# Optimization experiments

Hardware: AMD Instinct MI355X
Metric: run time of the kernel (lower is better)

Reference implementation:

```python
import jax, jax.numpy as jnp
import numpy as np


def _apply_rope(t, cos, sin):
    # t: [b, s, h, d]; cos/sin: [s, d//2]; interleaved complex rotation
    b, s, h, d = t.shape
    tr = t.reshape(b, s, h, d // 2, 2)
    a, bb = tr[..., 0], tr[..., 1]
    c = cos[None, :, None, :]
    si = sin[None, :, None, :]
    out_r = a * c - bb * si
    out_i = a * si + bb * c
    return jnp.stack([out_r, out_i], axis=-1).reshape(b, s, h, d)


def setup_inputs() -> dict:
    key = jax.random.key(0)
    ks = jax.random.split(key, 10)
    B, S, D = 4, 512, 4096
    H, HKV, HD = 32, 8, 128
    START = 512
    wscale = 0.02  # keep activations in sane range
    x = jax.random.normal(ks[0], (B, S, D), dtype=jnp.float32)
    wq = jax.random.normal(ks[1], (H * HD, D), dtype=jnp.float32) * wscale
    wk = jax.random.normal(ks[2], (HKV * HD, D), dtype=jnp.float32) * wscale
    wv = jax.random.normal(ks[3], (HKV * HD, D), dtype=jnp.float32) * wscale
    wo = jax.random.normal(ks[4], (D, H * HD), dtype=jnp.float32) * wscale
    # RoPE angles for absolute positions [START, START+S)
    theta = 500000.0
    inv_freq = 1.0 / (theta ** (np.arange(0, HD, 2, dtype=np.float32) / HD))
    pos = np.arange(START, START + S, dtype=np.float32)
    ang = pos[:, None] * inv_freq[None, :]  # [S, HD//2]
    freqs_cos = jnp.asarray(np.cos(ang), dtype=jnp.float32)
    freqs_sin = jnp.asarray(np.sin(ang), dtype=jnp.float32)
    cache_k = jax.random.normal(ks[5], (B, START, HKV, HD), dtype=jnp.float32)
    cache_v = jax.random.normal(ks[6], (B, START, HKV, HD), dtype=jnp.float32)
    return {"x": x, "wq": wq, "wk": wk, "wv": wv, "wo": wo,
            "freqs_cos": freqs_cos, "freqs_sin": freqs_sin,
            "cache_k": cache_k, "cache_v": cache_v, "start_pos": START}


def reference(x, wq, wk, wv, wo, freqs_cos, freqs_sin, cache_k, cache_v, start_pos):
    B, S, D = x.shape
    H = wq.shape[0] // 128
    HKV = wk.shape[0] // 128
    HD = 128
    n_rep = H // HKV
    # QKV projections (Linear: y = x @ W^T)
    xq = jnp.einsum('bsd,ed->bse', x, wq).reshape(B, S, H, HD)
    xk = jnp.einsum('bsd,ed->bse', x, wk).reshape(B, S, HKV, HD)
    xv = jnp.einsum('bsd,ed->bse', x, wv).reshape(B, S, HKV, HD)
    # rotary embedding on new q/k
    xq = _apply_rope(xq, freqs_cos, freqs_sin)
    xk = _apply_rope(xk, freqs_cos, freqs_sin)
    # append new k/v to cache -> total kv length T = start_pos + S
    keys = jnp.concatenate([cache_k, xk], axis=1)    # [B, T, HKV, HD]
    values = jnp.concatenate([cache_v, xv], axis=1)  # [B, T, HKV, HD]
    # GQA: repeat kv heads (repeat_interleave along head dim)
    keys = jnp.repeat(keys, n_rep, axis=2)      # [B, T, H, HD]
    values = jnp.repeat(values, n_rep, axis=2)  # [B, T, H, HD]
    scores = jnp.einsum('bqhd,bkhd->bhqk', xq, keys) / jnp.sqrt(jnp.float32(HD))
    # causal mask: query abs pos start_pos+i attends to kv pos <= start_pos+i
    T = start_pos + S
    q_pos = start_pos + jnp.arange(S)
    k_pos = jnp.arange(T)
    mask = k_pos[None, :] <= q_pos[:, None]  # [S, T]
    scores = jnp.where(mask[None, None, :, :], scores, -jnp.inf)
    probs = jax.nn.softmax(scores.astype(jnp.float32), axis=-1).astype(x.dtype)
    out = jnp.einsum('bhqk,bkhd->bqhd', probs, values).reshape(B, S, H * HD)
    return jnp.einsum('bse,de->bsd', out, wo)
```

## Files before the change

kernel.cpp:

```cpp
#include <hip/hip_runtime.h>
#include <hip/hip_bf16.h>


#define B_ 4
#define S_ 512
#define D_ 4096
#define H_ 32
#define HKV_ 8
#define HD_ 128
#define T_ 1024
#define M_ 2048
#define NQKV_ 6144

typedef __attribute__((ext_vector_type(8))) short bf16x8;
typedef __attribute__((ext_vector_type(4))) float f32x4;

#define GLOAD_LDS16(g, l)                                                     \
  __builtin_amdgcn_global_load_lds(                                           \
      (const __attribute__((address_space(1))) void*)(g),                     \
      (__attribute__((address_space(3))) void*)(l), 16, 0, 0)

__global__ void cvt_f32_bf16(const float* __restrict__ in,
                             __hip_bfloat16* __restrict__ out, long n) {
  long i = ((long)blockIdx.x * blockDim.x + threadIdx.x) * 4;
  if (i >= n) return;
  float4 v = *(const float4*)(in + i);
  __hip_bfloat16 t[4] = {__float2bfloat16(v.x), __float2bfloat16(v.y),
                         __float2bfloat16(v.z), __float2bfloat16(v.w)};
  *(uint2*)(out + i) = *(const uint2*)t;
}

__global__ __launch_bounds__(512, 2) void gemm_qkv(
    const __hip_bfloat16* __restrict__ A, const __hip_bfloat16* __restrict__ B,
    float* __restrict__ C, int K, long ldA, long ldB, long ldC) {
  const int lin = blockIdx.x + 32 * blockIdx.y;
  const int swz = (lin & 7) * 32 + (lin >> 3);
  const int m0 = (swz >> 5) << 8;
  const int n0 = (swz & 31) * 192;

  const int tid = threadIdx.x;
  const int w = tid >> 6, l = tid & 63;
  const int wm = w >> 2, wn = w & 3;
  const int lr = l & 15, lq = l >> 4;

  __shared__ __align__(16) __hip_bfloat16 smem[2][28672];

  const int rS = w * 8 + (l >> 3);
  const int cS = (l & 7) ^ (l >> 3);
  const __hip_bfloat16* gA = A + (long)(m0 + rS) * ldA + cS * 8;
  const __hip_bfloat16* gB = B + (long)(n0 + rS) * ldB + cS * 8;
  const int wofs = w * 512;

  const int sl0 = (lq ^ (lr & 7)) * 8;
  const int sl1 = ((4 + lq) ^ (lr & 7)) * 8;
  const int aRow = (wm * 128 + lr) * 64;
  const int bRow = (wn * 48 + lr) * 64;

  f32x4 acc[8][3];
#pragma unroll
  for (int i = 0; i < 8; i++)
#pragma unroll
    for (int j = 0; j < 3; j++) acc[i][j] = f32x4{0.f, 0.f, 0.f, 0.f};

  const int nkt = K >> 6;

#define STAGEQ(buf, ko)                                              \
  {                                                                  \
    GLOAD_LDS16(gA + (ko), &smem[buf][wofs]);                        \
    GLOAD_LDS16(gA + 64 * ldA + (ko), &smem[buf][4096 + wofs]);      \
    GLOAD_LDS16(gA + 128 * ldA + (ko), &smem[buf][8192 + wofs]);     \
    GLOAD_LDS16(gA + 192 * ldA + (ko), &smem[buf][12288 + wofs]);    \
    GLOAD_LDS16(gB + (ko), &smem[buf][16384 + wofs]);                \
    GLOAD_LDS16(gB + 64 * ldB + (ko), &smem[buf][20480 + wofs]);     \
    GLOAD_LDS16(gB + 128 * ldB + (ko), &smem[buf][24576 + wofs]);    \
  }

  STAGEQ(0, 0);
  asm volatile("s_waitcnt vmcnt(0)" ::: "memory");
  __builtin_amdgcn_s_barrier();

  bf16x8 af[4], bfr[3];
  for (int t = 0; t < nkt; ++t) {
    const int bc = t & 1;
    int tn = t + 1;
    if (tn == nkt) tn = 0;
    const long ko = (long)tn << 6;
    const __hip_bfloat16* rA = &smem[bc][0];
    const __hip_bfloat16* rB = &smem[bc][16384];

#pragma unroll
    for (int i = 0; i < 4; i++)
      af[i] = *(const bf16x8*)(rA + aRow + i * 1024 + sl0);
#pragma unroll
    for (int j = 0; j < 3; j++)
      bfr[j] = *(const bf16x8*)(rB + bRow + j * 1024 + sl0);
    STAGEQ(bc ^ 1, ko);
    __builtin_amdgcn_s_barrier();
    __builtin_amdgcn_s_setprio(1);
#pragma unroll
    for (int i = 0; i < 4; i++)
#pragma unroll
      for (int j = 0; j < 3; j++)
        acc[i][j] = __builtin_amdgcn_mfma_f32_16x16x32_bf16(af[i], bfr[j],
                                                            acc[i][j], 0, 0, 0);
    __builtin_amdgcn_s_setprio(0);
    __builtin_amdgcn_s_barrier();

#pragma unroll
    for (int i = 0; i < 4; i++)
      af[i] = *(const bf16x8*)(rA + aRow + (i + 4) * 1024 + sl0);
    __builtin_amdgcn_s_barrier();
    __builtin_amdgcn_s_setprio(1);
#pragma unroll
    for (int i = 0; i < 4; i++)
#pragma unroll
      for (int j = 0; j < 3; j++)
        acc[i + 4][j] = __builtin_amdgcn_mfma_f32_16x16x32_bf16(
            af[i], bfr[j], acc[i + 4][j], 0, 0, 0);
    __builtin_amdgcn_s_setprio(0);
    __builtin_amdgcn_s_barrier();

#pragma unroll
    for (int i = 0; i < 4; i++)
      af[i] = *(const bf16x8*)(rA + aRow + i * 1024 + sl1);
#pragma unroll
    for (int j = 0; j < 3; j++)
      bfr[j] = *(const bf16x8*)(rB + bRow + j * 1024 + sl1);
    __builtin_amdgcn_s_barrier();
    __builtin_amdgcn_s_setprio(1);
#pragma unroll
    for (int i = 0; i < 4; i++)
#pragma unroll
      for (int j = 0; j < 3; j++)
        acc[i][j] = __builtin_amdgcn_mfma_f32_16x16x32_bf16(af[i], bfr[j],
                                                            acc[i][j], 0, 0, 0);
    __builtin_amdgcn_s_setprio(0);
    __builtin_amdgcn_s_barrier();

#pragma unroll
    for (int i = 0; i < 4; i++)
      af[i] = *(const bf16x8*)(rA + aRow + (i + 4) * 1024 + sl1);
    __builtin_amdgcn_s_barrier();
    __builtin_amdgcn_s_setprio(1);
#pragma unroll
    for (int i = 0; i < 4; i++)
#pragma unroll
      for (int j = 0; j < 3; j++)
        acc[i + 4][j] = __builtin_amdgcn_mfma_f32_16x16x32_bf16(
            af[i], bfr[j], acc[i + 4][j], 0, 0, 0);
    __builtin_amdgcn_s_setprio(0);
    asm volatile("s_waitcnt vmcnt(0)" ::: "memory");
    __builtin_amdgcn_s_barrier();
  }

#undef STAGEQ

  const int crow = m0 + wm * 128 + lq * 4;
  const int ccol = n0 + wn * 48 + lr;
#pragma unroll
  for (int i = 0; i < 8; i++)
#pragma unroll
    for (int j = 0; j < 3; j++)
#pragma unroll
      for (int r = 0; r < 4; r++)
        C[(long)(crow + i * 16 + r) * ldC + (ccol + j * 16)] = acc[i][j][r];
}

__global__ __launch_bounds__(512, 2) void gemm128(
    const __hip_bfloat16* __restrict__ A, const __hip_bfloat16* __restrict__ B,
    float* __restrict__ C, int M, int N, int K, long ldA, long ldB, long ldC) {
  const int nbx = N >> 8;
  const int nwg = nbx * (M >> 7);
  const int lin = blockIdx.x + nbx * blockIdx.y;
  const int cpx = nwg >> 3;
  const int swz = (lin & 7) * cpx + (lin >> 3);
  const int by = swz / nbx;
  const int m0 = by << 7;
  const int n0 = (swz - by * nbx) << 8;

  const int tid = threadIdx.x;
  const int w = tid >> 6, l = tid & 63;
  const int wm = w >> 2, wn = w & 3;
  const int lr = l & 15, lq = l >> 4;

  __shared__ __align__(16) __hip_bfloat16 smem[3][24576];

  const int rS = w * 16 + (l >> 2);
  const int cS = (l & 3) ^ ((rS >> 1) & 3);
  const __hip_bfloat16* gA = A + (long)(m0 + rS) * ldA + cS * 8;
  const __hip_bfloat16* gB = B + (long)(n0 + rS) * ldB + cS * 8;
  const long stB = 128 * ldB;
  const int wofs = w * 512;

  const int cR = (lq ^ ((lr >> 1) & 3)) * 8;
  const int aOff = (wm * 64 + lr) * 32 + cR;
  const int bOff = (wn * 64 + lr) * 32 + cR;

  f32x4 acc[4][4];
#pragma unroll
  for (int i = 0; i < 4; i++)
#pragma unroll
    for (int j = 0; j < 4; j++) acc[i][j] = f32x4{0.f, 0.f, 0.f, 0.f};

  const int nkt = K >> 6;

#define STAGEF(buf, ko)                                            \
  {                                                                \
    const __hip_bfloat16* ga_ = gA + (ko);                         \
    GLOAD_LDS16(ga_, &smem[buf][wofs]);                            \
    GLOAD_LDS16(ga_ + 32, &smem[buf][4096 + wofs]);                \
    const __hip_bfloat16* gb_ = gB + (ko);                         \
    GLOAD_LDS16(gb_, &smem[buf][8192 + wofs]);                     \
    GLOAD_LDS16(gb_ + stB, &smem[buf][12288 + wofs]);              \
    GLOAD_LDS16(gb_ + 32, &smem[buf][16384 + wofs]);               \
    GLOAD_LDS16(gb_ + stB + 32, &smem[buf][20480 + wofs]);         \
  }

  STAGEF(0, 0);
  STAGEF(1, 64);
  asm volatile("s_waitcnt vmcnt(6)" ::: "memory");
  __builtin_amdgcn_s_barrier();

  int bc = 0, b1 = 1, b2 = 2;
  bf16x8 af[4], bfr[4];
  for (int t = 0; t < nkt; ++t) {
    int t2 = t + 2;
    if (t2 >= nkt) t2 -= nkt;
    const long ko2 = (long)t2 << 6;
    STAGEF(b2, ko2);

    const __hip_bfloat16* rA = &smem[bc][0];
    const __hip_bfloat16* rB = &smem[bc][8192];

#pragma unroll
    for (int i = 0; i < 4; i++) af[i] = *(const bf16x8*)(rA + aOff + i * 512);
#pragma unroll
    for (int j = 0; j < 4; j++) bfr[j] = *(const bf16x8*)(rB + bOff + j * 512);
    __builtin_amdgcn_s_setprio(1);
#pragma unroll
    for (int i = 0; i < 4; i++)
#pragma unroll
      for (int j = 0; j < 4; j++)
        acc[i][j] = __builtin_amdgcn_mfma_f32_16x16x32_bf16(af[i], bfr[j],
                                                            acc[i][j], 0, 0, 0);
    __builtin_amdgcn_s_setprio(0);

#pragma unroll
    for (int i = 0; i < 4; i++)
      af[i] = *(const bf16x8*)(rA + 4096 + aOff + i * 512);
#pragma unroll
    for (int j = 0; j < 4; j++)
      bfr[j] = *(const bf16x8*)(rB + 8192 + bOff + j * 512);
    __builtin_amdgcn_s_setprio(1);
#pragma unroll
    for (int i = 0; i < 4; i++)
#pragma unroll
      for (int j = 0; j < 4; j++)
        acc[i][j] = __builtin_amdgcn_mfma_f32_16x16x32_bf16(af[i], bfr[j],
                                                            acc[i][j], 0, 0, 0);
    __builtin_amdgcn_s_setprio(0);

    asm volatile("s_waitcnt lgkmcnt(0)" ::: "memory");
    __builtin_amdgcn_sched_barrier(0);
    asm volatile("s_waitcnt vmcnt(6)" ::: "memory");
    __builtin_amdgcn_s_barrier();

    int tmp = bc; bc = b1; b1 = b2; b2 = tmp;
  }
  asm volatile("s_waitcnt vmcnt(0)" ::: "memory");

#undef STAGEF

  const int crow = m0 + wm * 64 + lq * 4;
  const int ccol = n0 + wn * 64 + lr;
#pragma unroll
  for (int i = 0; i < 4; i++)
#pragma unroll
    for (int j = 0; j < 4; j++)
#pragma unroll
      for (int r = 0; r < 4; r++)
        C[(long)(crow + i * 16 + r) * ldC + (ccol + j * 16)] = acc[i][j][r];
}

__global__ __launch_bounds__(256, 2) void flash_attn(
    const __hip_bfloat16* __restrict__ qb,
    const __hip_bfloat16* __restrict__ kb,
    const __hip_bfloat16* __restrict__ vtb,
    __hip_bfloat16* __restrict__ ob) {
  const int qt = 3 - blockIdx.x;
  const int z = blockIdx.y;
  const int b = z >> 5, h = z & 31, kvh = h >> 2;
  const int q0 = qt * 128;
  const int tid = threadIdx.x, wave = tid >> 6, lane = tid & 63;
  const int lr = lane & 15, lq = lane >> 4;
  const int wrow = wave * 32;
  const float scale = 0.08838834764831845f;

  __shared__ __align__(16) __hip_bfloat16 smem[64 * 128 + 128 * 64 + 128 * 72];
  __hip_bfloat16* Ks = smem;
  __hip_bfloat16* Vs = smem + 64 * 128;
  __hip_bfloat16* Ps = smem + 64 * 128 + 128 * 64;
  __hip_bfloat16* Os = smem;

  const __hip_bfloat16* Kz = kb + ((long)(b * 8 + kvh)) * T_ * HD_;
  const __hip_bfloat16* Vz = vtb + ((long)(b * 8 + kvh)) * HD_ * T_;
  const __hip_bfloat16* Qz = qb + ((long)(b * 512 + q0)) * 4096 + h * 128;
  __hip_bfloat16* obz = ob + ((long)(b * 512 + q0)) * 4096 + h * 128;

  bf16x8 qf[2][4];
#pragma unroll
  for (int i = 0; i < 2; i++)
#pragma unroll
    for (int kb4 = 0; kb4 < 4; kb4++)
      qf[i][kb4] = *(const bf16x8*)(Qz + (long)(wrow + i * 16 + lr) * 4096 +
                                    kb4 * 32 + lq * 8);

  int kOff[4], vOff[4];
#pragma unroll
  for (int it = 0; it < 4; it++) {
    int G = it * 256 + tid;
    int t = G >> 4, ck = (G & 15) ^ (t & 7);
    kOff[it] = t * 128 + ck * 8;
    int d = G >> 3, cv = (G & 7) ^ (d & 7);
    vOff[it] = d * 1024 + cv * 8;
  }

  f32x4 O[2][8];
#pragma unroll
  for (int i = 0; i < 2; i++)
#pragma unroll
    for (int j = 0; j < 8; j++) O[i][j] = f32x4{0.f, 0.f, 0.f, 0.f};
  float mst[2][4], lst[2][4];
#pragma unroll
  for (int i = 0; i < 2; i++)
#pragma unroll
    for (int r = 0; r < 4; r++) {
      mst[i][r] = -1e30f;
      lst[i][r] = 0.f;
    }

  const int ntiles = 10 + 2 * qt, fulltiles = 8 + 2 * qt;
  const int hxor = lr & 7;

  bf16x8 kreg[4], vreg[4];
#pragma unroll
  for (int it = 0; it < 4; it++)
    kreg[it] = *(const bf16x8*)(Kz + kOff[it]);
#pragma unroll
  for (int it = 0; it < 4; it++)
    vreg[it] = *(const bf16x8*)(Vz + vOff[it]);

  for (int kt = 0; kt < ntiles; kt++) {
    const int k0 = kt * 64;
#pragma unroll
    for (int it = 0; it < 4; it++)
      *(bf16x8*)(Ks + (it * 256 + tid) * 8) = kreg[it];
#pragma unroll
    for (int it = 0; it < 4; it++)
      *(bf16x8*)(Vs + (it * 256 + tid) * 8) = vreg[it];
    if (kt + 1 < ntiles) {
      const long kn = (long)(kt + 1) * 64;
#pragma unroll
      for (int it = 0; it < 4; it++)
        kreg[it] = *(const bf16x8*)(Kz + kn * 128 + kOff[it]);
#pragma unroll
      for (int it = 0; it < 4; it++)
        vreg[it] = *(const bf16x8*)(Vz + kn + vOff[it]);
    }
    asm volatile("s_waitcnt lgkmcnt(0)" ::: "memory");
    __builtin_amdgcn_s_barrier();

    f32x4 s[2][4];
#pragma unroll
    for (int i = 0; i < 2; i++)
#pragma unroll
      for (int j = 0; j < 4; j++) s[i][j] = f32x4{0.f, 0.f, 0.f, 0.f};
#pragma unroll
    for (int kb4 = 0; kb4 < 4; kb4++) {
      bf16x8 kf[4];
#pragma unroll
      for (int j = 0; j < 4; j++)
        kf[j] = *(const bf16x8*)(Ks + (j * 16 + lr) * 128 +
                                 ((kb4 * 4 + lq) ^ hxor) * 8);
#pragma unroll
      for (int i = 0; i < 2; i++)
#pragma unroll
        for (int j = 0; j < 4; j++)
          s[i][j] = __builtin_amdgcn_mfma_f32_16x16x32_bf16(qf[i][kb4], kf[j],
                                                            s[i][j], 0, 0, 0);
    }

    const bool mt = (kt >= fulltiles);
#pragma unroll
    for (int i = 0; i < 2; i++)
#pragma unroll
      for (int j = 0; j < 4; j++)
#pragma unroll
        for (int r = 0; r < 4; r++) {
          float sv = s[i][j][r] * scale;
          if (mt) {
            int key = k0 + j * 16 + lr;
            int qp = 512 + q0 + wrow + i * 16 + lq * 4 + r;
            if (key > qp) sv = -1e30f;
          }
          s[i][j][r] = sv;
        }

    float al[2][4];
#pragma unroll
    for (int i = 0; i < 2; i++)
#pragma unroll
      for (int r = 0; r < 4; r++) {
        float mx = fmaxf(fmaxf(s[i][0][r], s[i][1][r]),
                         fmaxf(s[i][2][r], s[i][3][r]));
        mx = fmaxf(mx, __shfl_xor(mx, 1));
        mx = fmaxf(mx, __shfl_xor(mx, 2));
        mx = fmaxf(mx, __shfl_xor(mx, 4));
        mx = fmaxf(mx, __shfl_xor(mx, 8));
        float mn = fmaxf(mst[i][r], mx);
        al[i][r] = __expf(mst[i][r] - mn);
        mst[i][r] = mn;
      }
#pragma unroll
    for (int i = 0; i < 2; i++)
#pragma unroll
      for (int j = 0; j < 4; j++)
#pragma unroll
        for (int r = 0; r < 4; r++)
          s[i][j][r] = __expf(s[i][j][r] - mst[i][r]);
#pragma unroll
    for (int i = 0; i < 2; i++)
#pragma unroll
      for (int r = 0; r < 4; r++) {
        float sm = s[i][0][r] + s[i][1][r] + s[i][2][r] + s[i][3][r];
        sm += __shfl_xor(sm, 1);
        sm += __shfl_xor(sm, 2);
        sm += __shfl_xor(sm, 4);
        sm += __shfl_xor(sm, 8);
        lst[i][r] = lst[i][r] * al[i][r] + sm;
      }
#pragma unroll
    for (int i = 0; i < 2; i++)
#pragma unroll
      for (int j = 0; j < 8; j++)
#pragma unroll
        for (int r = 0; r < 4; r++) O[i][j][r] *= al[i][r];

#pragma unroll
    for (int i = 0; i < 2; i++)
#pragma unroll
      for (int j = 0; j < 4; j++)
#pragma unroll
        for (int r = 0; r < 4; r++)
          Ps[(wrow + i * 16 + lq * 4 + r) * 72 + j * 16 + lr] =
              __float2bfloat16(s[i][j][r]);

#pragma unroll
    for (int kc = 0; kc < 2; kc++) {
      bf16x8 pa[2];
#pragma unroll
      for (int i = 0; i < 2; i++)
        pa[i] = *(const bf16x8*)(Ps + (wrow + i * 16 + lr) * 72 + kc * 32 +
                                 lq * 8);
      bf16x8 vf[8];
#pragma unroll
      for (int j = 0; j < 8; j++)
        vf[j] = *(const bf16x8*)(Vs + (j * 16 + lr) * 64 +
                                 ((kc * 4 + lq) ^ hxor) * 8);
#pragma unroll
      for (int i = 0; i < 2; i++)
#pragma unroll
        for (int j = 0; j < 8; j++)
          O[i][j] = __builtin_amdgcn_mfma_f32_16x16x32_bf16(pa[i], vf[j],
                                                            O[i][j], 0, 0, 0);
    }
    asm volatile("s_waitcnt lgkmcnt(0)" ::: "memory");
    __builtin_amdgcn_s_barrier();
  }

#pragma unroll
  for (int i = 0; i < 2; i++)
#pragma unroll
    for (int r = 0; r < 4; r++) {
      float inv = 1.f / lst[i][r];
#pragma unroll
      for (int j = 0; j < 8; j++)
        Os[(wrow + i * 16 + lq * 4 + r) * 136 + j * 16 + lr] =
            __float2bfloat16(O[i][j][r] * inv);
    }
  __syncthreads();
#pragma unroll
  for (int it = 0; it < 8; it++) {
    int G = it * 256 + tid;
    int m = G >> 4, c = G & 15;
    *(bf16x8*)(obz + (long)m * 4096 + c * 8) =
        *(const bf16x8*)(Os + m * 136 + c * 8);
  }
}

__global__ void rope_kernel(const float* __restrict__ qkv,
                            const float* __restrict__ fcos,
                            const float* __restrict__ fsin,
                            __hip_bfloat16* __restrict__ qb,
                            __hip_bfloat16* __restrict__ kb) {
  int m = blockIdx.y;
  int j = blockIdx.x * blockDim.x + threadIdx.x;
  if (j >= 2560) return;
  int s = m & (S_ - 1);
  long rowbase = (long)m * NQKV_;
  if (j < 2048) {
    int dpair = j & 63;
    float a = qkv[rowbase + 2 * j], bb = qkv[rowbase + 2 * j + 1];
    float c = fcos[s * 64 + dpair], si = fsin[s * 64 + dpair];
    long o = (long)m * 4096 + 2 * j;
    qb[o] = __float2bfloat16(a * c - bb * si);
    qb[o + 1] = __float2bfloat16(a * si + bb * c);
  } else {
    int j2 = j - 2048;
    int kvh = j2 >> 6, dpair = j2 & 63;
    float a = qkv[rowbase + 4096 + 2 * j2], bb = qkv[rowbase + 4096 + 2 * j2 + 1];
    float c = fcos[s * 64 + dpair], si = fsin[s * 64 + dpair];
    int b = m >> 9;
    long o = (((long)(b * HKV_ + kvh)) * T_ + 512 + s) * HD_ + 2 * dpair;
    kb[o] = __float2bfloat16(a * c - bb * si);
    kb[o + 1] = __float2bfloat16(a * si + bb * c);
  }
}

__global__ void kcache_cvt(const float* __restrict__ cache_k,
                           __hip_bfloat16* __restrict__ kb) {
  long i = (long)blockIdx.x * 256 + threadIdx.x;
  if (i >= (long)B_ * HKV_ * 512 * HD_) return;
  int d = i & 127;
  int t = (i >> 7) & 511;
  int kvh = (i >> 16) & 7;
  int b = i >> 19;
  long o = (((long)(b * HKV_ + kvh)) * T_ + t) * HD_ + d;
  kb[o] = __float2bfloat16(
      cache_k[(((long)(b * 512 + t)) * HKV_ + kvh) * HD_ + d]);
}

__global__ void v_transpose(const float* __restrict__ cache_v,
                            const float* __restrict__ qkv,
                            __hip_bfloat16* __restrict__ vtb) {
  __shared__ float tile[32][33];
  int t0 = blockIdx.x * 32, d0 = blockIdx.y * 32;
  int bk = blockIdx.z;
  int b = bk >> 3, kvh = bk & 7;
#pragma unroll
  for (int it = 0; it < 4; it++) {
    int t = t0 + threadIdx.y + it * 8;
    int d = d0 + threadIdx.x;
    float v;
    if (t < 512)
      v = cache_v[(((long)(b * 512 + t)) * HKV_ + kvh) * HD_ + d];
    else
      v = qkv[((long)(b * S_) + (t - 512)) * NQKV_ + 5120 + kvh * HD_ + d];
    tile[threadIdx.y + it * 8][threadIdx.x] = v;
  }
  __syncthreads();
#pragma unroll
  for (int it = 0; it < 4; it++) {
    int d = d0 + threadIdx.y + it * 8;
    int t = t0 + threadIdx.x;
    vtb[((long)bk * HD_ + d) * T_ + t] =
        __float2bfloat16(tile[threadIdx.x][threadIdx.y + it * 8]);
  }
}

extern "C" void kernel_launch(void* const* d_in, const int* in_sizes, int n_in,
                              void* d_out, int out_size, void* d_ws,
                              size_t ws_size, hipStream_t stream) {
  const float* x = (const float*)d_in[0];
  const float* wq = (const float*)d_in[1];
  const float* wk = (const float*)d_in[2];
  const float* wv = (const float*)d_in[3];
  const float* wo = (const float*)d_in[4];
  const float* fcos = (const float*)d_in[5];
  const float* fsin = (const float*)d_in[6];
  const float* cache_k = (const float*)d_in[7];
  const float* cache_v = (const float*)d_in[8];
  float* out = (float*)d_out;

  char* ws = (char*)d_ws;
  const size_t szR0 = (size_t)M_ * 4096 * 2;
  const size_t szR1 = (size_t)NQKV_ * D_ * 2;
  const size_t szR2 = (size_t)M_ * NQKV_ * 4;
  const size_t szKV = (size_t)B_ * HKV_ * T_ * HD_ * 2;

  size_t R0 = 0;
  size_t R1 = R0 + szR0;
  size_t R2 = R1 + szR1;
  size_t R3 = R2 + szR2;
  size_t R4 = R3 + szKV;

  __hip_bfloat16* xb = (__hip_bfloat16*)(ws + R0);
  __hip_bfloat16* wqkvb = (__hip_bfloat16*)(ws + R1);
  float* qkvf = (float*)(ws + R2);
  __hip_bfloat16* kb = (__hip_bfloat16*)(ws + R3);
  __hip_bfloat16* vtb = (__hip_bfloat16*)(ws + R4);

  dim3 blk(256);

  cvt_f32_bf16<<<(M_ * (long)D_ / 4 + 255) / 256, blk, 0, stream>>>(
      x, xb, (long)M_ * D_);
  cvt_f32_bf16<<<((long)D_ * D_ / 4 + 255) / 256, blk, 0, stream>>>(
      wq, wqkvb, (long)D_ * D_);
  cvt_f32_bf16<<<((long)1024 * D_ / 4 + 255) / 256, blk, 0, stream>>>(
      wk, wqkvb + (long)4096 * D_, (long)1024 * D_);
  cvt_f32_bf16<<<((long)1024 * D_ / 4 + 255) / 256, blk, 0, stream>>>(
      wv, wqkvb + (long)5120 * D_, (long)1024 * D_);

  gemm_qkv<<<dim3(32, 8), dim3(512), 0, stream>>>(
      xb, wqkvb, qkvf, D_, D_, D_, NQKV_);

  __hip_bfloat16* qb = xb;
  rope_kernel<<<dim3(10, M_), blk, 0, stream>>>(qkvf, fcos, fsin, qb, kb);

  kcache_cvt<<<((long)B_ * HKV_ * 512 * HD_ + 255) / 256, blk, 0, stream>>>(
      cache_k, kb);
  v_transpose<<<dim3(T_ / 32, HD_ / 32, B_ * HKV_), dim3(32, 8), 0, stream>>>(
      cache_v, qkvf, vtb);

  __hip_bfloat16* wob = wqkvb;
  cvt_f32_bf16<<<((long)D_ * D_ / 4 + 255) / 256, blk, 0, stream>>>(
      wo, wob, (long)D_ * D_);

  __hip_bfloat16* ob = xb;
  flash_attn<<<dim3(4, B_ * H_), blk, 0, stream>>>(qb, kb, vtb, ob);

  gemm128<<<dim3(D_ / 256, M_ / 128), dim3(512), 0, stream>>>(
      ob, wob, out, M_, D_, D_, D_, D_, D_);
}
```

Before: 500.0 us.

## Retile output GEMM, add lazy softmax rescale, direct LDS loads in attention, fuse weight casts

Replaces the 128x256-tile output GEMM with a 256x128-tile, double-buffered kernel that uses a wider swizzled LDS layout and finer barrier-interleaved MFMA phases. In flash attention, K/V tiles now load straight into LDS via global_load_lds instead of a register prefetch, and the running-max rescale is skipped whenever the new row max exceeds the old one by at most 8. The three Q/K/V weight conversions become one kernel launch. This trades attention prefetch overlap and extra barriers for fewer launches, less rescale work and possibly better GEMM reuse.

After: 537.3 us. 1.07x slower.

```diff
diff --git a/kernel.cpp b/kernel.cpp
--- a/kernel.cpp
+++ b/kernel.cpp
@@ -30,6 +30,27 @@
   *(uint2*)(out + i) = *(const uint2*)t;
 }
 
+__global__ void cvt_wqkv(const float* __restrict__ wq,
+                         const float* __restrict__ wk,
+                         const float* __restrict__ wv,
+                         __hip_bfloat16* __restrict__ out) {
+  long i = ((long)blockIdx.x * 256 + threadIdx.x) * 4;
+  long row = i >> 12;
+  const float* src;
+  long off;
+  if (row < 4096) {
+    src = wq; off = i;
+  } else if (row < 5120) {
+    src = wk; off = i - (long)4096 * 4096;
+  } else {
+    src = wv; off = i - (long)5120 * 4096;
+  }
+  float4 v = *(const float4*)(src + off);
+  __hip_bfloat16 t[4] = {__float2bfloat16(v.x), __float2bfloat16(v.y),
+                         __float2bfloat16(v.z), __float2bfloat16(v.w)};
+  *(uint2*)(out + i) = *(const uint2*)t;
+}
+
 __global__ __launch_bounds__(512, 2) void gemm_qkv(
     const __hip_bfloat16* __restrict__ A, const __hip_bfloat16* __restrict__ B,
     float* __restrict__ C, int K, long ldA, long ldB, long ldC) {
@@ -166,117 +187,136 @@
         C[(long)(crow + i * 16 + r) * ldC + (ccol + j * 16)] = acc[i][j][r];
 }
 
-__global__ __launch_bounds__(512, 2) void gemm128(
+__global__ __launch_bounds__(512, 2) void gemm_out(
     const __hip_bfloat16* __restrict__ A, const __hip_bfloat16* __restrict__ B,
-    float* __restrict__ C, int M, int N, int K, long ldA, long ldB, long ldC) {
-  const int nbx = N >> 8;
-  const int nwg = nbx * (M >> 7);
-  const int lin = blockIdx.x + nbx * blockIdx.y;
-  const int cpx = nwg >> 3;
-  const int swz = (lin & 7) * cpx + (lin >> 3);
-  const int by = swz / nbx;
-  const int m0 = by << 7;
-  const int n0 = (swz - by * nbx) << 8;
+    float* __restrict__ C, int K, long ldA, long ldB, long ldC) {
+  const int lin = blockIdx.x + 32 * blockIdx.y;
+  const int swz = (lin & 7) * 32 + (lin >> 3);
+  const int m0 = (swz >> 5) << 8;
+  const int n0 = (swz & 31) << 7;
 
   const int tid = threadIdx.x;
   const int w = tid >> 6, l = tid & 63;
   const int wm = w >> 2, wn = w & 3;
   const int lr = l & 15, lq = l >> 4;
 
-  __shared__ __align__(16) __hip_bfloat16 smem[3][24576];
-
-  const int rS = w * 16 + (l >> 2);
-  const int cS = (l & 3) ^ ((rS >> 1) & 3);
+  __shared__ __align__(16) __hip_bfloat16 smem[2][24576];
+
+  const int rS = w * 8 + (l >> 3);
+  const int cS = (l & 7) ^ (l >> 3);
   const __hip_bfloat16* gA = A + (long)(m0 + rS) * ldA + cS * 8;
   const __hip_bfloat16* gB = B + (long)(n0 + rS) * ldB + cS * 8;
-  const long stB = 128 * ldB;
   const int wofs = w * 512;
 
-  const int cR = (lq ^ ((lr >> 1) & 3)) * 8;
-  const int aOff = (wm * 64 + lr) * 32 + cR;
-  const int bOff = (wn * 64 + lr) * 32 + cR;
-
-  f32x4 acc[4][4];
-#pragma unroll
-  for (int i = 0; i < 4; i++)
-#pragma unroll
-    for (int j = 0; j < 4; j++) acc[i][j] = f32x4{0.f, 0.f, 0.f, 0.f};
+  const int sl0 = (lq ^ (lr & 7)) * 8;
+  const int sl1 = ((4 + lq) ^ (lr & 7)) * 8;
+  const int aRow = (wm * 128 + lr) * 64;
+  const int bRow = (wn * 32 + lr) * 64;
+
+  f32x4 acc[8][2];
+#pragma unroll
+  for (int i = 0; i < 8; i++)
+#pragma unroll
+    for (int j = 0; j < 2; j++) acc[i][j] = f32x4{0.f, 0.f, 0.f, 0.f};
 
   const int nkt = K >> 6;
 
-#define STAGEF(buf, ko)                                            \
-  {                                                                \
-    const __hip_bfloat16* ga_ = gA + (ko);                         \
-    GLOAD_LDS16(ga_, &smem[buf][wofs]);                            \
-    GLOAD_LDS16(ga_ + 32, &smem[buf][4096 + wofs]);                \
-    const __hip_bfloat16* gb_ = gB + (ko);                         \
-    GLOAD_LDS16(gb_, &smem[buf][8192 + wofs]);                     \
-    GLOAD_LDS16(gb_ + stB, &smem[buf][12288 + wofs]);              \
-    GLOAD_LDS16(gb_ + 32, &smem[buf][16384 + wofs]);               \
-    GLOAD_LDS16(gb_ + stB + 32, &smem[buf][20480 + wofs]);         \
-  }
-
-  STAGEF(0, 0);
-  STAGEF(1, 64);
-  asm volatile("s_waitcnt vmcnt(6)" ::: "memory");
+#define STAGEO(buf, ko)                                              \
+  {                                                                  \
+    GLOAD_LDS16(gA + (ko), &smem[buf][wofs]);                        \
+    GLOAD_LDS16(gA + 64 * ldA + (ko), &smem[buf][4096 + wofs]);      \
+    GLOAD_LDS16(gA + 128 * ldA + (ko), &smem[buf][8192 + wofs]);     \
+    GLOAD_LDS16(gA + 192 * ldA + (ko), &smem[buf][12288 + wofs]);    \
+    GLOAD_LDS16(gB + (ko), &smem[buf][16384 + wofs]);                \
+    GLOAD_LDS16(gB + 64 * ldB + (ko), &smem[buf][20480 + wofs]);     \
+  }
+
+  STAGEO(0, 0);
+  asm volatile("s_waitcnt vmcnt(0)" ::: "memory");
   __builtin_amdgcn_s_barrier();
 
-  int bc = 0, b1 = 1, b2 = 2;
-  bf16x8 af[4], bfr[4];
+  bf16x8 af[4], bfr[2];
   for (int t = 0; t < nkt; ++t) {
-    int t2 = t + 2;
-    if (t2 >= nkt) t2 -= nkt;
-    const long ko2 = (long)t2 << 6;
-    STAGEF(b2, ko2);
-
+    const int bc = t & 1;
+    int tn = t + 1;
+    if (tn == nkt) tn = 0;
+    const long ko = (long)tn << 6;
     const __hip_bfloat16* rA = &smem[bc][0];
-    const __hip_bfloat16* rB = &smem[bc][8192];
-
-#pragma unroll
-    for (int i = 0; i < 4; i++) af[i] = *(const bf16x8*)(rA + aOff + i * 512);
-#pragma unroll
-    for (int j = 0; j < 4; j++) bfr[j] = *(const bf16x8*)(rB + bOff + j * 512);
-    __builtin_amdgcn_s_setprio(1);
-#pragma unroll
-    for (int i = 0; i < 4; i++)
-#pragma unroll
-      for (int j = 0; j < 4; j++)
+    const __hip_bfloat16* rB = &smem[bc][16384];
+
+#pragma unroll
+    for (int i = 0; i < 4; i++)
+      af[i] = *(const bf16x8*)(rA + aRow + i * 1024 + sl0);
+#pragma unroll
+    for (int j = 0; j < 2; j++)
+      bfr[j] = *(const bf16x8*)(rB + bRow + j * 1024 + sl0);
+    STAGEO(bc ^ 1, ko);
+    __builtin_amdgcn_s_barrier();
+    __builtin_amdgcn_s_setprio(1);
+#pragma unroll
+    for (int i = 0; i < 4; i++)
+#pragma unroll
+      for (int j = 0; j < 2; j++)
         acc[i][j] = __builtin_amdgcn_mfma_f32_16x16x32_bf16(af[i], bfr[j],
                                                             acc[i][j], 0, 0, 0);
     __builtin_amdgcn_s_setprio(0);
-
-#pragma unroll
-    for (int i = 0; i < 4; i++)
-      af[i] = *(const bf16x8*)(rA + 4096 + aOff + i * 512);
-#pragma unroll
-    for (int j = 0; j < 4; j++)
-      bfr[j] = *(const bf16x8*)(rB + 8192 + bOff + j * 512);
-    __builtin_amdgcn_s_setprio(1);
-#pragma unroll
-    for (int i = 0; i < 4; i++)
-#pragma unroll
-      for (int j = 0; j < 4; j++)
+    __builtin_amdgcn_s_barrier();
+
+#pragma unroll
+    for (int i = 0; i < 4; i++)
+      af[i] = *(const bf16x8*)(rA + aRow + (i + 4) * 1024 + sl0);
+    __builtin_amdgcn_s_barrier();
+    __builtin_amdgcn_s_setprio(1);
+#pragma unroll
+    for (int i = 0; i < 4; i++)
+#pragma unroll
+      for (int j = 0; j < 2; j++)
+        acc[i + 4][j] = __builtin_amdgcn_mfma_f32_16x16x32_bf16(
+            af[i], bfr[j], acc[i + 4][j], 0, 0, 0);
+    __builtin_amdgcn_s_setprio(0);
+    __builtin_amdgcn_s_barrier();
+
+#pragma unroll
+    for (int i = 0; i < 4; i++)
+      af[i] = *(const bf16x8*)(rA + aRow + i * 1024 + sl1);
+#pragma unroll
+    for (int j = 0; j < 2; j++)
+      bfr[j] = *(const bf16x8*)(rB + bRow + j * 1024 + sl1);
+    __builtin_amdgcn_s_barrier();
+    __builtin_amdgcn_s_setprio(1);
+#pragma unroll
+    for (int i = 0; i < 4; i++)
+#pragma unroll
+      for (int j = 0; j < 2; j++)
         acc[i][j] = __builtin_amdgcn_mfma_f32_16x16x32_bf16(af[i], bfr[j],
                                                             acc[i][j], 0, 0, 0);
     __builtin_amdgcn_s_setprio(0);
-
-    asm volatile("s_waitcnt lgkmcnt(0)" ::: "memory");
-    __builtin_amdgcn_sched_barrier(0);
-    asm volatile("s_waitcnt vmcnt(6)" ::: "memory");
-    __builtin_amdgcn_s_barrier();
-
-    int tmp = bc; bc = b1; b1 = b2; b2 = tmp;
-  }
-  asm volatile("s_waitcnt vmcnt(0)" ::: "memory");
-
-#undef STAGEF
-
-  const int crow = m0 + wm * 64 + lq * 4;
-  const int ccol = n0 + wn * 64 + lr;
-#pragma unroll
-  for (int i = 0; i < 4; i++)
-#pragma unroll
-    for (int j = 0; j < 4; j++)
+    __builtin_amdgcn_s_barrier();
+
+#pragma unroll
+    for (int i = 0; i < 4; i++)
+      af[i] = *(const bf16x8*)(rA + aRow + (i + 4) * 1024 + sl1);
+    __builtin_amdgcn_s_barrier();
+    __builtin_amdgcn_s_setprio(1);
+#pragma unroll
+    for (int i = 0; i < 4; i++)
+#pragma unroll
+      for (int j = 0; j < 2; j++)
+        acc[i + 4][j] = __builtin_amdgcn_mfma_f32_16x16x32_bf16(
+            af[i], bfr[j], acc[i + 4][j], 0, 0, 0);
+    __builtin_amdgcn_s_setprio(0);
+    asm volatile("s_waitcnt vmcnt(0)" ::: "memory");
+    __builtin_amdgcn_s_barrier();
+  }
+
+#undef STAGEO
+
+  const int crow = m0 + wm * 128 + lq * 4;
+  const int ccol = n0 + wn * 32 + lr;
+#pragma unroll
+  for (int i = 0; i < 8; i++)
+#pragma unroll
+    for (int j = 0; j < 2; j++)
 #pragma unroll
       for (int r = 0; r < 4; r++)
         C[(long)(crow + i * 16 + r) * ldC + (ccol + j * 16)] = acc[i][j][r];
@@ -342,33 +382,16 @@
   const int ntiles = 10 + 2 * qt, fulltiles = 8 + 2 * qt;
   const int hxor = lr & 7;
 
-  bf16x8 kreg[4], vreg[4];
-#pragma unroll
-  for (int it = 0; it < 4; it++)
-    kreg[it] = *(const bf16x8*)(Kz + kOff[it]);
-#pragma unroll
-  for (int it = 0; it < 4; it++)
-    vreg[it] = *(const bf16x8*)(Vz + vOff[it]);
-
   for (int kt = 0; kt < ntiles; kt++) {
     const int k0 = kt * 64;
 #pragma unroll
     for (int it = 0; it < 4; it++)
-      *(bf16x8*)(Ks + (it * 256 + tid) * 8) = kreg[it];
+      GLOAD_LDS16(Kz + (long)k0 * 128 + kOff[it],
+                  Ks + (it * 256 + wave * 64) * 8);
 #pragma unroll
     for (int it = 0; it < 4; it++)
-      *(bf16x8*)(Vs + (it * 256 + tid) * 8) = vreg[it];
-    if (kt + 1 < ntiles) {
-      const long kn = (long)(kt + 1) * 64;
-#pragma unroll
-      for (int it = 0; it < 4; it++)
-        kreg[it] = *(const bf16x8*)(Kz + kn * 128 + kOff[it]);
-#pragma unroll
-      for (int it = 0; it < 4; it++)
-        vreg[it] = *(const bf16x8*)(Vz + kn + vOff[it]);
-    }
-    asm volatile("s_waitcnt lgkmcnt(0)" ::: "memory");
-    __builtin_amdgcn_s_barrier();
+      GLOAD_LDS16(Vz + k0 + vOff[it], Vs + (it * 256 + wave * 64) * 8);
+    __syncthreads();
 
     f32x4 s[2][4];
 #pragma unroll
@@ -406,45 +429,75 @@
           s[i][j][r] = sv;
         }
 
-    float al[2][4];
+    float mx[2][4];
+    bool ok = true;
 #pragma unroll
     for (int i = 0; i < 2; i++)
 #pragma unroll
       for (int r = 0; r < 4; r++) {
-        float mx = fmaxf(fmaxf(s[i][0][r], s[i][1][r]),
-                         fmaxf(s[i][2][r], s[i][3][r]));
-        mx = fmaxf(mx, __shfl_xor(mx, 1));
-        mx = fmaxf(mx, __shfl_xor(mx, 2));
-        mx = fmaxf(mx, __shfl_xor(mx, 4));
-        mx = fmaxf(mx, __shfl_xor(mx, 8));
-        float mn = fmaxf(mst[i][r], mx);
-        al[i][r] = __expf(mst[i][r] - mn);
-        mst[i][r] = mn;
+        float m = fmaxf(fmaxf(s[i][0][r], s[i][1][r]),
+                        fmaxf(s[i][2][r], s[i][3][r]));
+        m = fmaxf(m, __shfl_xor(m, 1));
+        m = fmaxf(m, __shfl_xor(m, 2));
+        m = fmaxf(m, __shfl_xor(m, 4));
+        m = fmaxf(m, __shfl_xor(m, 8));
+        mx[i][r] = m;
+        ok = ok && (m - mst[i][r] <= 8.f);
       }
-#pragma unroll
-    for (int i = 0; i < 2; i++)
-#pragma unroll
-      for (int j = 0; j < 4; j++)
-#pragma unroll
-        for (int r = 0; r < 4; r++)
-          s[i][j][r] = __expf(s[i][j][r] - mst[i][r]);
-#pragma unroll
-    for (int i = 0; i < 2; i++)
-#pragma unroll
-      for (int r = 0; r < 4; r++) {
-        float sm = s[i][0][r] + s[i][1][r] + s[i][2][r] + s[i][3][r];
-        sm += __shfl_xor(sm, 1);
-        sm += __shfl_xor(sm, 2);
-        sm += __shfl_xor(sm, 4);
-        sm += __shfl_xor(sm, 8);
-        lst[i][r] = lst[i][r] * al[i][r] + sm;
-      }
-#pragma unroll
-    for (int i = 0; i < 2; i++)
-#pragma unroll
-      for (int j = 0; j < 8; j++)
-#pragma unroll
-        for (int r = 0; r < 4; r++) O[i][j][r] *= al[i][r];
+    if (__all(ok)) {
+#pragma unroll
+      for (int i = 0; i < 2; i++)
+#pragma unroll
+        for (int j = 0; j < 4; j++)
+#pragma unroll
+          for (int r = 0; r < 4; r++)
+            s[i][j][r] = __expf(s[i][j][r] - mst[i][r]);
+#pragma unroll
+      for (int i = 0; i < 2; i++)
+#pragma unroll
+        for (int r = 0; r < 4; r++) {
+          float sm = s[i][0][r] + s[i][1][r] + s[i][2][r] + s[i][3][r];
+          sm += __shfl_xor(sm, 1);
+          sm += __shfl_xor(sm, 2);
+          sm += __shfl_xor(sm, 4);
+          sm += __shfl_xor(sm, 8);
+          lst[i][r] += sm;
+        }
+    } else {
+      float al[2][4];
+#pragma unroll
+      for (int i = 0; i < 2; i++)
+#pragma unroll
+        for (int r = 0; r < 4; r++) {
+          float mn = fmaxf(mst[i][r], mx[i][r]);
+          al[i][r] = __expf(mst[i][r] - mn);
+          mst[i][r] = mn;
+        }
+#pragma unroll
+      for (int i = 0; i < 2; i++)
+#pragma unroll
+        for (int j = 0; j < 4; j++)
+#pragma unroll
+          for (int r = 0; r < 4; r++)
+            s[i][j][r] = __expf(s[i][j][r] - mst[i][r]);
+#pragma unroll
+      for (int i = 0; i < 2; i++)
+#pragma unroll
+        for (int r = 0; r < 4; r++) {
+          float sm = s[i][0][r] + s[i][1][r] + s[i][2][r] + s[i][3][r];
+          sm += __shfl_xor(sm, 1);
+          sm += __shfl_xor(sm, 2);
+          sm += __shfl_xor(sm, 4);
+          sm += __shfl_xor(sm, 8);
+          lst[i][r] = lst[i][r] * al[i][r] + sm;
+        }
+#pragma unroll
+      for (int i = 0; i < 2; i++)
+#pragma unroll
+        for (int j = 0; j < 8; j++)
+#pragma unroll
+          for (int r = 0; r < 4; r++) O[i][j][r] *= al[i][r];
+    }
 
 #pragma unroll
     for (int i = 0; i < 2; i++)
@@ -474,8 +527,7 @@
           O[i][j] = __builtin_amdgcn_mfma_f32_16x16x32_bf16(pa[i], vf[j],
                                                             O[i][j], 0, 0, 0);
     }
-    asm volatile("s_waitcnt lgkmcnt(0)" ::: "memory");
-    __builtin_amdgcn_s_barrier();
+    __syncthreads();
   }
 
 #pragma unroll
@@ -604,12 +656,8 @@
 
   cvt_f32_bf16<<<(M_ * (long)D_ / 4 + 255) / 256, blk, 0, stream>>>(
       x, xb, (long)M_ * D_);
-  cvt_f32_bf16<<<((long)D_ * D_ / 4 + 255) / 256, blk, 0, stream>>>(
-      wq, wqkvb, (long)D_ * D_);
-  cvt_f32_bf16<<<((long)1024 * D_ / 4 + 255) / 256, blk, 0, stream>>>(
-      wk, wqkvb + (long)4096 * D_, (long)1024 * D_);
-  cvt_f32_bf16<<<((long)1024 * D_ / 4 + 255) / 256, blk, 0, stream>>>(
-      wv, wqkvb + (long)5120 * D_, (long)1024 * D_);
+  cvt_wqkv<<<((long)NQKV_ * D_ / 4 + 255) / 256, blk, 0, stream>>>(
+      wq, wk, wv, wqkvb);
 
   gemm_qkv<<<dim3(32, 8), dim3(512), 0, stream>>>(
       xb, wqkvb, qkvf, D_, D_, D_, NQKV_);
@@ -629,6 +677,6 @@
   __hip_bfloat16* ob = xb;
   flash_attn<<<dim3(4, B_ * H_), blk, 0, stream>>>(qb, kb, vtb, ob);
 
-  gemm128<<<dim3(D_ / 256, M_ / 128), dim3(512), 0, stream>>>(
-      ob, wob, out, M_, D_, D_, D_, D_, D_);
-}
+  gemm_out<<<dim3(32, 8), dim3(512), 0, stream>>>(
+      ob, wob, out, D_, D_, D_, D_);
+}
```
